# Kernel tuning notes

Measured on AMD Instinct MI355X. Metric: run time of the kernel, lower is better.

Reference implementation:

```python
import jax, jax.numpy as jnp
import numpy as np

N = 50000      # nodes
E = 800000     # edges
B = 512        # graphs in batch
DRNL = 64      # drnl_dim (feature_dim = 0)
H = 256        # hidden


def setup_inputs() -> dict:
    key = jax.random.key(0)
    ks = jax.random.split(key, 12)
    x = jax.random.normal(ks[0], (N, DRNL), jnp.float32)
    edge_index = jax.random.randint(ks[1], (2, E), 0, N)
    batch_vec = jnp.sort(jax.random.randint(ks[2], (N,), 0, B))
    u_idx = jax.random.randint(ks[3], (B,), 0, N)
    v_idx = jax.random.randint(ks[4], (B,), 0, N)

    def glorot(k, shp):
        scale = jnp.sqrt(2.0 / (shp[0] + shp[1]))
        return (jax.random.normal(k, shp, jnp.float32) * scale).astype(jnp.float32)

    W0 = glorot(ks[5], (DRNL, H)); b0 = jnp.zeros((H,), jnp.float32)
    W1 = glorot(ks[6], (H, H));    b1 = jnp.zeros((H,), jnp.float32)
    W2 = glorot(ks[7], (H, H));    b2 = jnp.zeros((H,), jnp.float32)
    Wm1 = glorot(ks[8], (3 * H, H)); bm1 = jnp.zeros((H,), jnp.float32)
    Wm2 = glorot(ks[9], (H, 1));     bm2 = jnp.zeros((1,), jnp.float32)
    return dict(x=x, edge_index=edge_index, batch_vec=batch_vec,
                u_idx=u_idx, v_idx=v_idx,
                W0=W0, b0=b0, W1=W1, b1=b1, W2=W2, b2=b2,
                Wm1=Wm1, bm1=bm1, Wm2=Wm2, bm2=bm2)


def _gcn_encode(x, src, dst, Ws, bs):
    # Standard GCN: h' = D^-1/2 (A + I) D^-1/2 h W + b, ReLU between layers.
    n = x.shape[0]
    loop = jnp.arange(n)
    src2 = jnp.concatenate([src, loop])  # add self-loops
    dst2 = jnp.concatenate([dst, loop])
    deg = jax.ops.segment_sum(jnp.ones_like(dst2, x.dtype), dst2, num_segments=n)
    dis = jax.lax.rsqrt(jnp.maximum(deg, 1.0))          # D^-1/2
    norm = dis[src2] * dis[dst2]                         # per-edge norm [E+N]

    h = x
    for i, (W, b) in enumerate(zip(Ws, bs)):
        msg = h[src2] * norm[:, None]                    # gather + scale
        agg = jax.ops.segment_sum(msg, dst2, num_segments=n)
        h = agg @ W + b
        if i < len(Ws) - 1:
            h = jax.nn.relu(h)
    return h


def reference(x, edge_index, batch_vec, u_idx, v_idx,
              W0, b0, W1, b1, W2, b2, Wm1, bm1, Wm2, bm2):
    src, dst = edge_index[0], edge_index[1]
    h = _gcn_encode(x, src, dst, (W0, W1, W2), (b0, b1, b2))   # [N, H]

    # global_mean_pool over batch_vec -> [B, H]
    cnt = jax.ops.segment_sum(jnp.ones((h.shape[0],), h.dtype), batch_vec,
                              num_segments=B)
    g = jax.ops.segment_sum(h, batch_vec, num_segments=B) / \
        jnp.maximum(cnt, 1.0)[:, None]

    # concat [g, h[u], h[v]] -> MLP -> [B] logits
    z = jnp.concatenate([g, h[u_idx], h[v_idx]], axis=1)       # [B, 3H]
    z = jax.nn.relu(z @ Wm1 + bm1)
    return (z @ Wm2 + bm2).squeeze(-1)
```

## Files before the change

kernel.cpp:

```cpp
#include <hip/hip_runtime.h>
#include <hip/hip_bf16.h>
#include <stdint.h>

#ifndef DRNL
#define DRNL 64
#define HDIM 256
#endif

#define CHUNK 4096
#define BCAP 3072

typedef __attribute__((ext_vector_type(4))) float f32x4;
typedef __attribute__((ext_vector_type(8))) _Float16 f16x8;

__device__ __forceinline__ void async16(void* lds, const void* g) {
    __builtin_amdgcn_global_load_lds(
        (const __attribute__((address_space(1))) void*)g,
        (__attribute__((address_space(3))) void*)(char*)lds, 16, 0, 0);
}

__device__ __forceinline__ int imin(int a, int b) { return a < b ? a : b; }

__global__ __launch_bounds__(256) void k_misc(
    const int* __restrict__ batch,
    const float* __restrict__ x,
    const float* __restrict__ W0, const float* __restrict__ W1,
    const float* __restrict__ W2,
    int* __restrict__ gstart,
    _Float16* __restrict__ x16,
    _Float16* __restrict__ W0t, _Float16* __restrict__ W1t,
    _Float16* __restrict__ W2t,
    int N, int B) {
    const int gsz = gridDim.x * 256;
    const int gid0 = blockIdx.x * 256 + threadIdx.x;

    for (int i = gid0; i < (DRNL + 2 * HDIM) * 256; i += gsz) {
        int b = i >> 8, c = i & 255;
        const float* W; _Float16* T; int k, K;
        if (b < DRNL)            { W = W0; T = W0t; k = b;              K = DRNL; }
        else if (b < DRNL + 256) { W = W1; T = W1t; k = b - DRNL;       K = HDIM; }
        else                     { W = W2; T = W2t; k = b - DRNL - 256; K = HDIM; }
        int KT = K >> 5;
        int cg = c >> 6, ct = (c >> 4) & 3, cl = c & 15;
        int kt = k >> 5, qq = (k >> 3) & 3, j = k & 7;
        int lane = (qq << 4) | cl;
        T[(((size_t)(cg * KT + kt) * 4 + ct) * 64 + lane) * 8 + j] =
            (_Float16)W[(size_t)k * 256 + c];
    }

    for (int i = gid0; i < N * DRNL; i += gsz) x16[i] = (_Float16)x[i];

    for (int i = gid0; i <= N; i += gsz) {
        if (i == 0) {
            int b0 = batch[0];
            for (int b = 0; b <= b0; ++b) gstart[b] = 0;
        } else if (i == N) {
            int bl = batch[N - 1];
            for (int b = bl + 1; b <= B; ++b) gstart[b] = N;
        } else {
            int bp = batch[i - 1], bc = batch[i];
            if (bc != bp)
                for (int b = bp + 1; b <= bc; ++b) gstart[b] = i;
        }
    }
}

__global__ __launch_bounds__(256) void k_hist(const int* __restrict__ dst,
                                              int* __restrict__ ghist,
                                              int E, int P, int SH, int NBUCK) {
    __shared__ int h[512];
    int tid = threadIdx.x, p = blockIdx.x;
    for (int i = tid; i < NBUCK; i += 256) h[i] = 0;
    __syncthreads();
    int e0 = p * CHUNK, e1 = imin(e0 + CHUNK, E);
    for (int e = e0 + tid; e < e1; e += 256)
        atomicAdd(&h[dst[e] >> SH], 1);
    __syncthreads();
    for (int b = tid; b < NBUCK; b += 256)
        ghist[(size_t)b * P + p] = h[b];
}

__global__ __launch_bounds__(256) void k_gbase(int* __restrict__ ghist,
                                               int* __restrict__ btot, int P) {
    __shared__ int s[256];
    int b = blockIdx.x, tid = threadIdx.x;
    int* row = ghist + (size_t)b * P;
    int carry = 0;
    for (int base = 0; base < P; base += 256) {
        int idx = base + tid;
        int v = (idx < P) ? row[idx] : 0;
        s[tid] = v;
        __syncthreads();
        for (int o = 1; o < 256; o <<= 1) {
            int t = (tid >= o) ? s[tid - o] : 0;
            __syncthreads();
            s[tid] += t;
            __syncthreads();
        }
        if (idx < P) row[idx] = carry + s[tid] - v;
        carry += s[255];
        __syncthreads();
    }
    if (tid == 0) btot[b] = carry;
}

__global__ __launch_bounds__(256) void k_btscan(const int* __restrict__ btot,
                                                int* __restrict__ bbase,
                                                int* __restrict__ rowptr,
                                                int NBUCK, int N, int E) {
    __shared__ int s[256];
    int tid = threadIdx.x;
    int carry = 0;
    for (int base = 0; base < NBUCK; base += 256) {
        int idx = base + tid;
        int v = (idx < NBUCK) ? btot[idx] : 0;
        s[tid] = v;
        __syncthreads();
        for (int o = 1; o < 256; o <<= 1) {
            int t = (tid >= o) ? s[tid - o] : 0;
            __syncthreads();
            s[tid] += t;
            __syncthreads();
        }
        if (idx < NBUCK) bbase[idx] = carry + s[tid] - v;
        carry += s[255];
        __syncthreads();
    }
    if (tid == 0) { bbase[NBUCK] = E; rowptr[N] = E; }
}

__global__ __launch_bounds__(256) void k_scatter(const int* __restrict__ src,
                                                 const int* __restrict__ dst,
                                                 const int* __restrict__ ghist,
                                                 const int* __restrict__ bbase,
                                                 int* __restrict__ tmp,
                                                 int E, int P, int SH, int NBUCK) {
    __shared__ int base[512];
    int p = blockIdx.x, tid = threadIdx.x;
    for (int b = tid; b < NBUCK; b += 256)
        base[b] = bbase[b] + ghist[(size_t)b * P + p];
    __syncthreads();
    int e0 = p * CHUNK, e1 = imin(e0 + CHUNK, E);
    int msk = (1 << SH) - 1;
    for (int e = e0 + tid; e < e1; e += 256) {
        int d = dst[e];
        int r = atomicAdd(&base[d >> SH], 1);
        tmp[r] = (src[e] << SH) | (d & msk);
    }
}

__global__ __launch_bounds__(256) void k_bsort(const int* __restrict__ tmp,
                                               const int* __restrict__ bbase,
                                               int* __restrict__ col,
                                               int* __restrict__ rowptr,
                                               float* __restrict__ dis,
                                               _Float16* __restrict__ x16,
                                               int SH, int N) {
    __shared__ int cnt[512];
    __shared__ int off[512];
    __shared__ int sscan[256];
    __shared__ int eL[BCAP];
    __shared__ unsigned short rnk[BCAP];
    __shared__ int sL[BCAP];
    int b = blockIdx.x, tid = threadIdx.x;
    int nodes = 1 << SH, node0 = b << SH, msk = nodes - 1;
    int lo = bbase[b], hi = bbase[b + 1], m = hi - lo;
    bool fast = (m <= BCAP);

    for (int i = tid; i < nodes; i += 256) cnt[i] = 0;
    __syncthreads();
    if (fast) {
        for (int i = tid; i < m; i += 256) {
            int v = tmp[lo + i];
            eL[i] = v;
            rnk[i] = (unsigned short)atomicAdd(&cnt[v & msk], 1);
        }
    } else {
        for (int i = tid; i < m; i += 256)
            atomicAdd(&cnt[tmp[lo + i] & msk], 1);
    }
    __syncthreads();
    int carry = 0;
    for (int base = 0; base < nodes; base += 256) {
        int idx = base + tid;
        int v = (idx < nodes) ? cnt[idx] : 0;
        sscan[tid] = v;
        __syncthreads();
        for (int o = 1; o < 256; o <<= 1) {
            int t = (tid >= o) ? sscan[tid - o] : 0;
            __syncthreads();
            sscan[tid] += t;
            __syncthreads();
        }
        if (idx < nodes) off[idx] = carry + sscan[tid] - v;
        carry += sscan[255];
        __syncthreads();
    }
    for (int i = tid; i < nodes; i += 256) {
        int node = node0 + i;
        if (node < N) {
            rowptr[node] = lo + off[i];
            dis[node]    = rsqrtf((float)cnt[i] + 1.f);
        }
    }
    int rlim = imin(nodes, N - node0);
    for (int u = tid; u < rlim * 8; u += 256) {
        int r = u >> 3, c = u & 7;
        float d = rsqrtf((float)cnt[r] + 1.f);
        f16x8* xv = (f16x8*)(x16 + (size_t)(node0 + r) * 64);
        f16x8 v = xv[c];
        f16x8 o;
#pragma unroll
        for (int k = 0; k < 8; ++k) o[k] = (_Float16)((float)v[k] * d);
        xv[c] = o;
    }
    __syncthreads();
    if (fast) {
        for (int i = tid; i < m; i += 256) {
            int v = eL[i];
            sL[off[v & msk] + rnk[i]] = v >> SH;
        }
        __syncthreads();
        for (int i = tid; i < m; i += 256) col[lo + i] = sL[i];
    } else {
        for (int i = tid; i < nodes; i += 256) cnt[i] = 0;
        __syncthreads();
        for (int i = tid; i < m; i += 256) {
            int v = tmp[lo + i];
            int d = v & msk;
            int r = atomicAdd(&cnt[d], 1);
            col[lo + off[d] + r] = v >> SH;
        }
    }
}

template <int FBLK>
__global__ __launch_bounds__(256) void k_agg(const _Float16* __restrict__ hs,
                                             const float* __restrict__ dis,
                                             const int* __restrict__ rowptr,
                                             const int* __restrict__ col,
                                             _Float16* __restrict__ A16, int N) {
    int node_wg, f;
    if constexpr (FBLK == 4) {
        int wg = blockIdx.x;
        int xcd = wg & 7;
        f = xcd >> 1;
        int half = xcd & 1;
        int NH = gridDim.x >> 3;
        node_wg = half * NH + (wg >> 3);
    } else {
        node_wg = blockIdx.x;
        f = 0;
    }
    int lane = threadIdx.x & 63;
    int wv = threadIdx.x >> 6;
    int oct = lane >> 3;
    int fl = lane & 7;
    int gw = node_wg * 32 + wv * 8 + oct;
    bool valid = gw < N;
    int gwc = valid ? gw : N - 1;
    const size_t boff = (size_t)f * ((size_t)N * 64);
    const f16x8* hv = (const f16x8*)(hs + boff);
    float acc[8];
#pragma unroll
    for (int k = 0; k < 8; ++k) acc[k] = 0.f;

    int e0 = rowptr[gwc];
    int e1 = valid ? rowptr[gwc + 1] : e0;
    int j = e0;
    while (__any(j < e1)) {
        bool a0 = j < e1, a1 = j + 1 < e1, a2 = j + 2 < e1, a3 = j + 3 < e1;
        int s0 = col[a0 ? j : 0];
        int s1 = col[a1 ? j + 1 : 0];
        int s2 = col[a2 ? j + 2 : 0];
        int s3 = col[a3 ? j + 3 : 0];
        float m0 = a0 ? 1.f : 0.f, m1 = a1 ? 1.f : 0.f;
        float m2 = a2 ? 1.f : 0.f, m3 = a3 ? 1.f : 0.f;
        f16x8 v0 = hv[(size_t)s0 * 8 + fl];
        f16x8 v1 = hv[(size_t)s1 * 8 + fl];
        f16x8 v2 = hv[(size_t)s2 * 8 + fl];
        f16x8 v3 = hv[(size_t)s3 * 8 + fl];
#pragma unroll
        for (int k = 0; k < 8; ++k) acc[k] += m0 * (float)v0[k];
#pragma unroll
        for (int k = 0; k < 8; ++k) acc[k] += m1 * (float)v1[k];
#pragma unroll
        for (int k = 0; k < 8; ++k) acc[k] += m2 * (float)v2[k];
#pragma unroll
        for (int k = 0; k < 8; ++k) acc[k] += m3 * (float)v3[k];
        j += 4;
    }

    float dn = dis[gwc];
    f16x8 hsv = hv[(size_t)gwc * 8 + fl];
    f16x8 o;
#pragma unroll
    for (int k = 0; k < 8; ++k)
        o[k] = (_Float16)((acc[k] + (float)hsv[k]) * dn);
    if (valid)
        __builtin_nontemporal_store(
            o, (f16x8*)(A16 + boff + (size_t)gw * 64 + fl * 8));
}

template <int K, int OUT_RELU, int SCALE>
__global__ __launch_bounds__(256, 1) void k_wgemm(const _Float16* __restrict__ A,
                                                  const _Float16* __restrict__ Wf,
                                                  const float* __restrict__ bias,
                                                  const float* __restrict__ dis,
                                                  _Float16* __restrict__ outh, int n) {
    constexpr int KT  = K / 32;
    constexpr int NFB = K / 64;
    constexpr int NI  = NFB * 2;
    constexpr int STG = NFB * 1024;
    __shared__ _Float16 sAll[4 * (STG + 1024)];

    const int tid  = threadIdx.x;
    const int lane = tid & 63;
    const int wv   = tid >> 6;
    const int c15  = lane & 15;
    const int q    = lane >> 4;
    const int row0 = blockIdx.x * 64;
    const size_t bstride = (size_t)n * 64;
    _Float16* sbuf = sAll + wv * (STG + 1024);
    _Float16* sO   = sbuf + STG;
    _Float16* ob   = outh + (size_t)wv * bstride;

    f16x8 wf[4][KT];
    const _Float16* wp = Wf + ((size_t)wv * KT * 4 * 64 + lane) * 8;
#pragma unroll
    for (int kt = 0; kt < KT; ++kt)
#pragma unroll
        for (int ct = 0; ct < 4; ++ct)
            wf[ct][kt] = *(const f16x8*)(wp + (size_t)((kt * 4 + ct) * 64) * 8);

    float bvl = bias[(wv << 6) + lane];
    float bv[4];
#pragma unroll
    for (int ct = 0; ct < 4; ++ct) bv[ct] = __shfl(bvl, (ct << 4) + c15);

    float dsv[4][4];
    if (SCALE) {
        float dvl = dis[imin(row0 + lane, n - 1)];
#pragma unroll
        for (int st = 0; st < 4; ++st)
#pragma unroll
            for (int r = 0; r < 4; ++r)
                dsv[st][r] = __shfl(dvl, (st << 4) + (q << 2) + r);
    }

#pragma unroll
    for (int st = 0; st < 4; ++st) {
        const int r0 = row0 + (st << 4);
#pragma unroll
        for (int i = 0; i < NI; ++i) {
            int s   = (i << 6) + lane;
            int fb  = s >> 7;
            int row = (s >> 3) & 15;
            int ch  = (s & 7) ^ (row & 7);
            int gr  = imin(r0 + row, n - 1);
            async16(sbuf + (size_t)s * 8,
                    A + (size_t)fb * bstride + (size_t)gr * 64 + ch * 8);
        }
        asm volatile("s_waitcnt vmcnt(0)" ::: "memory");
        __builtin_amdgcn_sched_barrier(0);

        f16x8 af[KT];
#pragma unroll
        for (int kt = 0; kt < KT; ++kt) {
            int off = (kt >> 1) * 1024 + c15 * 64 +
                      ((((kt & 1) * 4 + q) ^ (c15 & 7)) * 8);
            af[kt] = *(const f16x8*)(sbuf + off);
        }

        f32x4 acc[4];
#pragma unroll
        for (int ct = 0; ct < 4; ++ct) acc[ct] = (f32x4)0.f;
#pragma unroll
        for (int kt = 0; kt < KT; ++kt)
#pragma unroll
            for (int ct = 0; ct < 4; ++ct)
                acc[ct] = __builtin_amdgcn_mfma_f32_16x16x32_f16(
                    af[kt], wf[ct][kt], acc[ct], 0, 0, 0);

#pragma unroll
        for (int ct = 0; ct < 4; ++ct) {
#pragma unroll
            for (int r = 0; r < 4; ++r) {
                float v = acc[ct][r] + bv[ct];
                if (OUT_RELU) v = fmaxf(v, 0.f);
                if (SCALE) v *= dsv[st][r];
                int row = (q << 2) + r;
                int colx = (ct << 4) + c15;
                int sw = (((colx >> 3) ^ (row & 7)) << 3) | (colx & 7);
                sO[row * 64 + sw] = (_Float16)v;
            }
        }
#pragma unroll
        for (int ps = 0; ps < 2; ++ps) {
            int u = (ps << 6) + lane;
            int rr = u >> 3, ch2 = u & 7;
            f16x8 vv = *(const f16x8*)(sO + rr * 64 + ((ch2 ^ (rr & 7)) << 3));
            if (r0 + rr < n)
                *(f16x8*)(ob + (size_t)(r0 + rr) * 64 + ch2 * 8) = vv;
        }
    }
}

__global__ __launch_bounds__(256) void k_head(const _Float16* __restrict__ h,
                                              const int* __restrict__ gstart,
                                              const int* __restrict__ u,
                                              const int* __restrict__ v,
                                              const float* __restrict__ Wm1,
                                              const float* __restrict__ bm1,
                                              const float* __restrict__ Wm2,
                                              const float* __restrict__ bm2,
                                              float* __restrict__ out, int N) {
    int b = blockIdx.x;
    int t = threadIdx.x;
    __shared__ float z[3 * HDIM];
    __shared__ float red[4];
    const _Float16* hb = h + (size_t)(t >> 6) * ((size_t)N * 64) + (t & 63);
    int s = gstart[b], e = gstart[b + 1];
    float pa = 0.f;
    int i = s;
    for (; i + 3 < e; i += 4) {
        float a0 = (float)hb[(size_t)i * 64];
        float a1 = (float)hb[(size_t)(i + 1) * 64];
        float a2 = (float)hb[(size_t)(i + 2) * 64];
        float a3 = (float)hb[(size_t)(i + 3) * 64];
        pa += (a0 + a1) + (a2 + a3);
    }
    for (; i < e; ++i) pa += (float)hb[(size_t)i * 64];
    z[t]            = pa / fmaxf((float)(e - s), 1.f);
    z[HDIM + t]     = (float)hb[(size_t)u[b] * 64];
    z[2 * HDIM + t] = (float)hb[(size_t)v[b] * 64];
    __syncthreads();
    float acc[8];
#pragma unroll
    for (int k = 0; k < 8; ++k) acc[k] = 0.f;
    for (int k = 0; k < 3 * HDIM; k += 8) {
#pragma unroll
        for (int jj = 0; jj < 8; ++jj)
            acc[jj] = fmaf(z[k + jj], Wm1[(size_t)(k + jj) * HDIM + t], acc[jj]);
    }
    float sum = (((acc[0] + acc[1]) + (acc[2] + acc[3])) +
                 ((acc[4] + acc[5]) + (acc[6] + acc[7]))) + bm1[t];
    float hid = fmaxf(sum, 0.f);
    float p = hid * Wm2[t];
    for (int off = 32; off; off >>= 1) p += __shfl_down(p, off);
    if ((t & 63) == 0) red[t >> 6] = p;
    __syncthreads();
    if (t == 0) out[b] = red[0] + red[1] + red[2] + red[3] + bm2[0];
}

extern "C" void kernel_launch(void* const* d_in, const int* in_sizes, int n_in,
                              void* d_out, int out_size, void* d_ws, size_t ws_size,
                              hipStream_t stream) {
    const float* x    = (const float*)d_in[0];
    const int*   ei   = (const int*)d_in[1];
    const int*   batc = (const int*)d_in[2];
    const int*   uidx = (const int*)d_in[3];
    const int*   vidx = (const int*)d_in[4];
    const float* W0   = (const float*)d_in[5];
    const float* b0   = (const float*)d_in[6];
    const float* W1   = (const float*)d_in[7];
    const float* b1   = (const float*)d_in[8];
    const float* W2   = (const float*)d_in[9];
    const float* b2   = (const float*)d_in[10];
    const float* Wm1  = (const float*)d_in[11];
    const float* bm1  = (const float*)d_in[12];
    const float* Wm2  = (const float*)d_in[13];
    const float* bm2  = (const float*)d_in[14];
    float* out = (float*)d_out;

    const int N = in_sizes[0] / DRNL;
    const int E = in_sizes[1] / 2;
    const int B = in_sizes[3];
    const int* src = ei;
    const int* dst = ei + E;

    int SH = 7;
    while (((N + (1 << SH) - 1) >> SH) > 512) ++SH;
    const int NBUCK = (N + (1 << SH) - 1) >> SH;
    const int P = (E + CHUNK - 1) / CHUNK;

    char* w = (char*)d_ws;
    size_t off = 0;
    auto carve = [&](size_t bytes) {
        void* p = w + off;
        off = (off + bytes + 255) & ~(size_t)255;
        return p;
    };
    int*       rowptr = (int*)carve((size_t)(N + 1) * 4);
    int*       colA   = (int*)carve((size_t)E * 4);
    float*     dis    = (float*)carve((size_t)N * 4);
    int*       gstart = (int*)carve((size_t)(B + 1) * 4);
    _Float16*  A16    = (_Float16*)carve((size_t)N * HDIM * 2);
    _Float16*  h16    = (_Float16*)carve((size_t)N * HDIM * 2);
    _Float16*  x16    = (_Float16*)carve((size_t)N * DRNL * 2);
    _Float16*  W0t    = (_Float16*)carve((size_t)DRNL * HDIM * 2);
    _Float16*  W1t    = (_Float16*)carve((size_t)HDIM * HDIM * 2);
    _Float16*  W2t    = (_Float16*)carve((size_t)HDIM * HDIM * 2);
    int*       ghist  = (int*)carve((size_t)NBUCK * P * 4);
    int*       btot   = (int*)carve(512 * 4);
    int*       bbase  = (int*)carve(513 * 4);
    int*       tmpE   = (int*)carve((size_t)E * 4);
    (void)ws_size;

    k_misc<<<1024, 256, 0, stream>>>(batc, x, W0, W1, W2, gstart,
                                     x16, W0t, W1t, W2t, N, B);
    k_hist<<<P, 256, 0, stream>>>(dst, ghist, E, P, SH, NBUCK);
    k_gbase<<<NBUCK, 256, 0, stream>>>(ghist, btot, P);
    k_btscan<<<1, 256, 0, stream>>>(btot, bbase, rowptr, NBUCK, N, E);
    k_scatter<<<P, 256, 0, stream>>>(src, dst, ghist, bbase, tmpE, E, P, SH, NBUCK);
    k_bsort<<<NBUCK, 256, 0, stream>>>(tmpE, bbase, colA, rowptr, dis, x16, SH, N);

    int gemmb = (N + 63) / 64;
    int NB = (N + 31) / 32;
    int NH = (NB + 1) / 2;
    int aggb4 = 8 * NH;

    k_agg<1><<<NB, 256, 0, stream>>>(x16, dis, rowptr, colA, A16, N);
    k_wgemm<DRNL, 1, 1><<<gemmb, 256, 0, stream>>>(A16, W0t, b0, dis, h16, N);
    k_agg<4><<<aggb4, 256, 0, stream>>>(h16, dis, rowptr, colA, A16, N);
    k_wgemm<HDIM, 1, 1><<<gemmb, 256, 0, stream>>>(A16, W1t, b1, dis, h16, N);
    k_agg<4><<<aggb4, 256, 0, stream>>>(h16, dis, rowptr, colA, A16, N);
    k_wgemm<HDIM, 0, 0><<<gemmb, 256, 0, stream>>>(A16, W2t, b2, dis, h16, N);

    k_head<<<B, 256, 0, stream>>>(h16, gstart, uidx, vidx, Wm1, bm1, Wm2, bm2, out, N);
}
```

Baseline: 294.4 us.

## Fuse histogram into misc kernel, dynamic node scheduling in agg, double-buffer GEMM

Merges the edge histogram kernel into k_misc as extra blocks, removing one launch, and vectorizes the x-to-fp16 conversion to 16-byte loads and stores. The aggregation kernel now gives each workgroup 128 nodes and hands them out through an LDS atomic counter, so octets that finish short adjacency lists pick up new nodes instead of idling. The weight GEMM swaps its per-wave LDS staging for a shared double-buffered async load that prefetches the next 16-row stage while the current one is computed, and raises launch bounds to allow two blocks per CU. In exchange it adds barriers and atomics, and register pressure may grow under the new occupancy target.

```diff
diff --git a/kernel.cpp b/kernel.cpp
--- a/kernel.cpp
+++ b/kernel.cpp
@@ -30,9 +30,28 @@
     _Float16* __restrict__ x16,
     _Float16* __restrict__ W0t, _Float16* __restrict__ W1t,
     _Float16* __restrict__ W2t,
+    const int* __restrict__ dst, int* __restrict__ ghist,
+    int E, int P, int SH, int NBUCK,
     int N, int B) {
-    const int gsz = gridDim.x * 256;
-    const int gid0 = blockIdx.x * 256 + threadIdx.x;
+    const int tid = threadIdx.x;
+
+    if (blockIdx.x < P) {
+        __shared__ int h[512];
+        int p = blockIdx.x;
+        for (int i = tid; i < NBUCK; i += 256) h[i] = 0;
+        __syncthreads();
+        int e0 = p * CHUNK, e1 = imin(e0 + CHUNK, E);
+        for (int e = e0 + tid; e < e1; e += 256)
+            atomicAdd(&h[dst[e] >> SH], 1);
+        __syncthreads();
+        for (int b = tid; b < NBUCK; b += 256)
+            ghist[(size_t)b * P + p] = h[b];
+        return;
+    }
+
+    const int bid  = blockIdx.x - P;
+    const int gsz  = (gridDim.x - P) * 256;
+    const int gid0 = bid * 256 + tid;
 
     for (int i = gid0; i < (DRNL + 2 * HDIM) * 256; i += gsz) {
         int b = i >> 8, c = i & 255;
@@ -48,7 +67,20 @@
             (_Float16)W[(size_t)k * 256 + c];
     }
 
-    for (int i = gid0; i < N * DRNL; i += gsz) x16[i] = (_Float16)x[i];
+    {
+        const float4* x4 = (const float4*)x;
+        f16x8* xv = (f16x8*)x16;
+        int tot = N * DRNL / 8;
+        for (int i = gid0; i < tot; i += gsz) {
+            float4 a = x4[2 * i], b2 = x4[2 * i + 1];
+            f16x8 o;
+            o[0] = (_Float16)a.x;  o[1] = (_Float16)a.y;
+            o[2] = (_Float16)a.z;  o[3] = (_Float16)a.w;
+            o[4] = (_Float16)b2.x; o[5] = (_Float16)b2.y;
+            o[6] = (_Float16)b2.z; o[7] = (_Float16)b2.w;
+            xv[i] = o;
+        }
+    }
 
     for (int i = gid0; i <= N; i += gsz) {
         if (i == 0) {
@@ -63,21 +95,6 @@
                 for (int b = bp + 1; b <= bc; ++b) gstart[b] = i;
         }
     }
-}
-
-__global__ __launch_bounds__(256) void k_hist(const int* __restrict__ dst,
-                                              int* __restrict__ ghist,
-                                              int E, int P, int SH, int NBUCK) {
-    __shared__ int h[512];
-    int tid = threadIdx.x, p = blockIdx.x;
-    for (int i = tid; i < NBUCK; i += 256) h[i] = 0;
-    __syncthreads();
-    int e0 = p * CHUNK, e1 = imin(e0 + CHUNK, E);
-    for (int e = e0 + tid; e < e1; e += 256)
-        atomicAdd(&h[dst[e] >> SH], 1);
-    __syncthreads();
-    for (int b = tid; b < NBUCK; b += 256)
-        ghist[(size_t)b * P + p] = h[b];
 }
 
 __global__ __launch_bounds__(256) void k_gbase(int* __restrict__ ghist,
@@ -240,6 +257,7 @@
                                              const int* __restrict__ rowptr,
                                              const int* __restrict__ col,
                                              _Float16* __restrict__ A16, int N) {
+    __shared__ int cur;
     int node_wg, f;
     if constexpr (FBLK == 4) {
         int wg = blockIdx.x;
@@ -252,67 +270,85 @@
         node_wg = blockIdx.x;
         f = 0;
     }
-    int lane = threadIdx.x & 63;
-    int wv = threadIdx.x >> 6;
-    int oct = lane >> 3;
-    int fl = lane & 7;
-    int gw = node_wg * 32 + wv * 8 + oct;
-    bool valid = gw < N;
-    int gwc = valid ? gw : N - 1;
+    if (threadIdx.x == 0) cur = 32;
+    __syncthreads();
+    const int base = node_wg * 128;
+    const int lim  = imin(128, N - base);
+    if (lim <= 0) return;
+    const int lane  = threadIdx.x & 63;
+    const int fl    = lane & 7;
+    const int obase = lane & 56;
     const size_t boff = (size_t)f * ((size_t)N * 64);
     const f16x8* hv = (const f16x8*)(hs + boff);
+
+    int myn = threadIdx.x >> 3;
+    bool active = myn < lim;
+    int gn = base + (active ? myn : 0);
+    int j = 0, e1 = 0;
+    if (active) { j = rowptr[gn]; e1 = rowptr[gn + 1]; }
     float acc[8];
 #pragma unroll
     for (int k = 0; k < 8; ++k) acc[k] = 0.f;
 
-    int e0 = rowptr[gwc];
-    int e1 = valid ? rowptr[gwc + 1] : e0;
-    int j = e0;
-    while (__any(j < e1)) {
-        bool a0 = j < e1, a1 = j + 1 < e1, a2 = j + 2 < e1, a3 = j + 3 < e1;
-        int s0 = col[a0 ? j : 0];
-        int s1 = col[a1 ? j + 1 : 0];
-        int s2 = col[a2 ? j + 2 : 0];
-        int s3 = col[a3 ? j + 3 : 0];
-        float m0 = a0 ? 1.f : 0.f, m1 = a1 ? 1.f : 0.f;
-        float m2 = a2 ? 1.f : 0.f, m3 = a3 ? 1.f : 0.f;
-        f16x8 v0 = hv[(size_t)s0 * 8 + fl];
-        f16x8 v1 = hv[(size_t)s1 * 8 + fl];
-        f16x8 v2 = hv[(size_t)s2 * 8 + fl];
-        f16x8 v3 = hv[(size_t)s3 * 8 + fl];
-#pragma unroll
-        for (int k = 0; k < 8; ++k) acc[k] += m0 * (float)v0[k];
-#pragma unroll
-        for (int k = 0; k < 8; ++k) acc[k] += m1 * (float)v1[k];
-#pragma unroll
-        for (int k = 0; k < 8; ++k) acc[k] += m2 * (float)v2[k];
-#pragma unroll
-        for (int k = 0; k < 8; ++k) acc[k] += m3 * (float)v3[k];
-        j += 4;
-    }
-
-    float dn = dis[gwc];
-    f16x8 hsv = hv[(size_t)gwc * 8 + fl];
-    f16x8 o;
-#pragma unroll
-    for (int k = 0; k < 8; ++k)
-        o[k] = (_Float16)((acc[k] + (float)hsv[k]) * dn);
-    if (valid)
-        __builtin_nontemporal_store(
-            o, (f16x8*)(A16 + boff + (size_t)gw * 64 + fl * 8));
+    while (__any(active)) {
+        if (active) {
+            bool a0 = j < e1, a1 = j + 1 < e1, a2 = j + 2 < e1, a3 = j + 3 < e1;
+            int s0 = col[a0 ? j : 0];
+            int s1 = col[a1 ? j + 1 : 0];
+            int s2 = col[a2 ? j + 2 : 0];
+            int s3 = col[a3 ? j + 3 : 0];
+            float m0 = a0 ? 1.f : 0.f, m1 = a1 ? 1.f : 0.f;
+            float m2 = a2 ? 1.f : 0.f, m3 = a3 ? 1.f : 0.f;
+            f16x8 v0 = hv[(size_t)s0 * 8 + fl];
+            f16x8 v1 = hv[(size_t)s1 * 8 + fl];
+            f16x8 v2 = hv[(size_t)s2 * 8 + fl];
+            f16x8 v3 = hv[(size_t)s3 * 8 + fl];
+#pragma unroll
+            for (int k = 0; k < 8; ++k) acc[k] += m0 * (float)v0[k];
+#pragma unroll
+            for (int k = 0; k < 8; ++k) acc[k] += m1 * (float)v1[k];
+#pragma unroll
+            for (int k = 0; k < 8; ++k) acc[k] += m2 * (float)v2[k];
+#pragma unroll
+            for (int k = 0; k < 8; ++k) acc[k] += m3 * (float)v3[k];
+            j += 4;
+            if (j >= e1) {
+                float dn = dis[gn];
+                f16x8 hsv = hv[(size_t)gn * 8 + fl];
+                f16x8 o;
+#pragma unroll
+                for (int k = 0; k < 8; ++k)
+                    o[k] = (_Float16)((acc[k] + (float)hsv[k]) * dn);
+                __builtin_nontemporal_store(
+                    o, (f16x8*)(A16 + boff + (size_t)gn * 64 + fl * 8));
+#pragma unroll
+                for (int k = 0; k < 8; ++k) acc[k] = 0.f;
+                int nn = 0;
+                if (fl == 0) nn = atomicAdd(&cur, 1);
+                nn = __shfl(nn, obase);
+                if (nn < lim) {
+                    myn = nn; gn = base + myn;
+                    j = rowptr[gn]; e1 = rowptr[gn + 1];
+                } else {
+                    active = false;
+                }
+            }
+        }
+    }
 }
 
 template <int K, int OUT_RELU, int SCALE>
-__global__ __launch_bounds__(256, 1) void k_wgemm(const _Float16* __restrict__ A,
+__global__ __launch_bounds__(256, 2) void k_wgemm(const _Float16* __restrict__ A,
                                                   const _Float16* __restrict__ Wf,
                                                   const float* __restrict__ bias,
                                                   const float* __restrict__ dis,
                                                   _Float16* __restrict__ outh, int n) {
-    constexpr int KT  = K / 32;
-    constexpr int NFB = K / 64;
-    constexpr int NI  = NFB * 2;
-    constexpr int STG = NFB * 1024;
-    __shared__ _Float16 sAll[4 * (STG + 1024)];
+    constexpr int KT    = K / 32;
+    constexpr int CPR   = K / 8;
+    constexpr int SLOTS = 16 * CPR;
+    constexpr int SHW   = 16 * K;
+    __shared__ _Float16 sA[2 * SHW];
+    __shared__ _Float16 sOut[4 * 16 * 64];
 
     const int tid  = threadIdx.x;
     const int lane = tid & 63;
@@ -321,9 +357,28 @@
     const int q    = lane >> 4;
     const int row0 = blockIdx.x * 64;
     const size_t bstride = (size_t)n * 64;
-    _Float16* sbuf = sAll + wv * (STG + 1024);
-    _Float16* sO   = sbuf + STG;
-    _Float16* ob   = outh + (size_t)wv * bstride;
+    _Float16* sO = sOut + wv * (16 * 64);
+    _Float16* ob = outh + (size_t)wv * bstride;
+
+    auto stage = [&](int b, int st) {
+        const int r0 = row0 + (st << 4);
+        _Float16* dstp = sA + b * SHW;
+#pragma unroll
+        for (int i = 0; i < (SLOTS + 255) / 256; ++i) {
+            int s = (i << 8) + tid;
+            if (SLOTS % 256 == 0 || s < SLOTS) {
+                int row = s / CPR;
+                int chs = s % CPR;
+                int cg  = chs ^ (row & 7);
+                int gr  = imin(r0 + row, n - 1);
+                async16(dstp + (size_t)s * 8,
+                        A + (size_t)(cg >> 3) * bstride + (size_t)gr * 64 +
+                            (cg & 7) * 8);
+            }
+        }
+    };
+
+    stage(0, 0);
 
     f16x8 wf[4][KT];
     const _Float16* wp = Wf + ((size_t)wv * KT * 4 * 64 + lane) * 8;
@@ -348,28 +403,20 @@
                 dsv[st][r] = __shfl(dvl, (st << 4) + (q << 2) + r);
     }
 
+    asm volatile("s_waitcnt vmcnt(0)" ::: "memory");
+    __builtin_amdgcn_sched_barrier(0);
+    __builtin_amdgcn_s_barrier();
+
 #pragma unroll
     for (int st = 0; st < 4; ++st) {
-        const int r0 = row0 + (st << 4);
-#pragma unroll
-        for (int i = 0; i < NI; ++i) {
-            int s   = (i << 6) + lane;
-            int fb  = s >> 7;
-            int row = (s >> 3) & 15;
-            int ch  = (s & 7) ^ (row & 7);
-            int gr  = imin(r0 + row, n - 1);
-            async16(sbuf + (size_t)s * 8,
-                    A + (size_t)fb * bstride + (size_t)gr * 64 + ch * 8);
-        }
-        asm volatile("s_waitcnt vmcnt(0)" ::: "memory");
-        __builtin_amdgcn_sched_barrier(0);
-
+        if (st < 3) stage((st + 1) & 1, st + 1);
+
+        const _Float16* buf = sA + (st & 1) * SHW;
         f16x8 af[KT];
 #pragma unroll
         for (int kt = 0; kt < KT; ++kt) {
-            int off = (kt >> 1) * 1024 + c15 * 64 +
-                      ((((kt & 1) * 4 + q) ^ (c15 & 7)) * 8);
-            af[kt] = *(const f16x8*)(sbuf + off);
+            int cg = kt * 4 + q;
+            af[kt] = *(const f16x8*)(buf + c15 * K + ((cg ^ (c15 & 7)) * 8));
         }
 
         f32x4 acc[4];
@@ -382,6 +429,7 @@
                 acc[ct] = __builtin_amdgcn_mfma_f32_16x16x32_f16(
                     af[kt], wf[ct][kt], acc[ct], 0, 0, 0);
 
+        const int r0 = row0 + (st << 4);
 #pragma unroll
         for (int ct = 0; ct < 4; ++ct) {
 #pragma unroll
@@ -402,6 +450,12 @@
             f16x8 vv = *(const f16x8*)(sO + rr * 64 + ((ch2 ^ (rr & 7)) << 3));
             if (r0 + rr < n)
                 *(f16x8*)(ob + (size_t)(r0 + rr) * 64 + ch2 * 8) = vv;
+        }
+
+        if (st < 3) {
+            asm volatile("s_waitcnt vmcnt(2)" ::: "memory");
+            __builtin_amdgcn_sched_barrier(0);
+            __builtin_amdgcn_s_barrier();
         }
     }
 }
@@ -507,20 +561,20 @@
     int*       tmpE   = (int*)carve((size_t)E * 4);
     (void)ws_size;
 
-    k_misc<<<1024, 256, 0, stream>>>(batc, x, W0, W1, W2, gstart,
-                                     x16, W0t, W1t, W2t, N, B);
-    k_hist<<<P, 256, 0, stream>>>(dst, ghist, E, P, SH, NBUCK);
+    k_misc<<<P + 1024, 256, 0, stream>>>(batc, x, W0, W1, W2, gstart,
+                                         x16, W0t, W1t, W2t,
+                                         dst, ghist, E, P, SH, NBUCK, N, B);
     k_gbase<<<NBUCK, 256, 0, stream>>>(ghist, btot, P);
     k_btscan<<<1, 256, 0, stream>>>(btot, bbase, rowptr, NBUCK, N, E);
     k_scatter<<<P, 256, 0, stream>>>(src, dst, ghist, bbase, tmpE, E, P, SH, NBUCK);
     k_bsort<<<NBUCK, 256, 0, stream>>>(tmpE, bbase, colA, rowptr, dis, x16, SH, N);
 
     int gemmb = (N + 63) / 64;
-    int NB = (N + 31) / 32;
-    int NH = (NB + 1) / 2;
+    int NB128 = (N + 127) / 128;
+    int NH = (NB128 + 1) / 2;
     int aggb4 = 8 * NH;
 
-    k_agg<1><<<NB, 256, 0, stream>>>(x16, dis, rowptr, colA, A16, N);
+    k_agg<1><<<NB128, 256, 0, stream>>>(x16, dis, rowptr, colA, A16, N);
     k_wgemm<DRNL, 1, 1><<<gemmb, 256, 0, stream>>>(A16, W0t, b0, dis, h16, N);
     k_agg<4><<<aggb4, 256, 0, stream>>>(h16, dis, rowptr, colA, A16, N);
     k_wgemm<HDIM, 1, 1><<<gemmb, 256, 0, stream>>>(A16, W1t, b1, dis, h16, N);
```

Result: slower. 322.6 us (+9.6%).

## Merge histogram into misc kernel, vectorize x cast, unroll gather by 8

Applied to the files above, without the earlier changes.

Folds the dst-bucket histogram kernel into the misc preprocessing kernel as extra leading blocks, removing one launch and letting the two independent jobs run side by side. The fp32-to-fp16 conversion of x is vectorised to move eight elements per thread iteration. The aggregation loop now issues eight neighbour gathers per step instead of four, for more memory-level parallelism. The cost is higher register use and more masked wasted loads on low-degree nodes.

```diff
diff --git a/kernel.cpp b/kernel.cpp
--- a/kernel.cpp
+++ b/kernel.cpp
@@ -30,9 +30,28 @@
     _Float16* __restrict__ x16,
     _Float16* __restrict__ W0t, _Float16* __restrict__ W1t,
     _Float16* __restrict__ W2t,
+    const int* __restrict__ dst, int* __restrict__ ghist,
+    int E, int P, int SH, int NBUCK,
     int N, int B) {
-    const int gsz = gridDim.x * 256;
-    const int gid0 = blockIdx.x * 256 + threadIdx.x;
+    const int tid = threadIdx.x;
+
+    if (blockIdx.x < P) {
+        __shared__ int h[512];
+        int p = blockIdx.x;
+        for (int i = tid; i < NBUCK; i += 256) h[i] = 0;
+        __syncthreads();
+        int e0 = p * CHUNK, e1 = imin(e0 + CHUNK, E);
+        for (int e = e0 + tid; e < e1; e += 256)
+            atomicAdd(&h[dst[e] >> SH], 1);
+        __syncthreads();
+        for (int b = tid; b < NBUCK; b += 256)
+            ghist[(size_t)b * P + p] = h[b];
+        return;
+    }
+
+    const int bid  = blockIdx.x - P;
+    const int gsz  = (gridDim.x - P) * 256;
+    const int gid0 = bid * 256 + tid;
 
     for (int i = gid0; i < (DRNL + 2 * HDIM) * 256; i += gsz) {
         int b = i >> 8, c = i & 255;
@@ -48,7 +67,20 @@
             (_Float16)W[(size_t)k * 256 + c];
     }
 
-    for (int i = gid0; i < N * DRNL; i += gsz) x16[i] = (_Float16)x[i];
+    {
+        const float4* x4 = (const float4*)x;
+        f16x8* xv = (f16x8*)x16;
+        int tot = N * DRNL / 8;
+        for (int i = gid0; i < tot; i += gsz) {
+            float4 a = x4[2 * i], b2 = x4[2 * i + 1];
+            f16x8 o;
+            o[0] = (_Float16)a.x;  o[1] = (_Float16)a.y;
+            o[2] = (_Float16)a.z;  o[3] = (_Float16)a.w;
+            o[4] = (_Float16)b2.x; o[5] = (_Float16)b2.y;
+            o[6] = (_Float16)b2.z; o[7] = (_Float16)b2.w;
+            xv[i] = o;
+        }
+    }
 
     for (int i = gid0; i <= N; i += gsz) {
         if (i == 0) {
@@ -63,21 +95,6 @@
                 for (int b = bp + 1; b <= bc; ++b) gstart[b] = i;
         }
     }
-}
-
-__global__ __launch_bounds__(256) void k_hist(const int* __restrict__ dst,
-                                              int* __restrict__ ghist,
-                                              int E, int P, int SH, int NBUCK) {
-    __shared__ int h[512];
-    int tid = threadIdx.x, p = blockIdx.x;
-    for (int i = tid; i < NBUCK; i += 256) h[i] = 0;
-    __syncthreads();
-    int e0 = p * CHUNK, e1 = imin(e0 + CHUNK, E);
-    for (int e = e0 + tid; e < e1; e += 256)
-        atomicAdd(&h[dst[e] >> SH], 1);
-    __syncthreads();
-    for (int b = tid; b < NBUCK; b += 256)
-        ghist[(size_t)b * P + p] = h[b];
 }
 
 __global__ __launch_bounds__(256) void k_gbase(int* __restrict__ ghist,
@@ -269,26 +286,24 @@
     int e1 = valid ? rowptr[gwc + 1] : e0;
     int j = e0;
     while (__any(j < e1)) {
-        bool a0 = j < e1, a1 = j + 1 < e1, a2 = j + 2 < e1, a3 = j + 3 < e1;
-        int s0 = col[a0 ? j : 0];
-        int s1 = col[a1 ? j + 1 : 0];
-        int s2 = col[a2 ? j + 2 : 0];
-        int s3 = col[a3 ? j + 3 : 0];
-        float m0 = a0 ? 1.f : 0.f, m1 = a1 ? 1.f : 0.f;
-        float m2 = a2 ? 1.f : 0.f, m3 = a3 ? 1.f : 0.f;
-        f16x8 v0 = hv[(size_t)s0 * 8 + fl];
-        f16x8 v1 = hv[(size_t)s1 * 8 + fl];
-        f16x8 v2 = hv[(size_t)s2 * 8 + fl];
-        f16x8 v3 = hv[(size_t)s3 * 8 + fl];
-#pragma unroll
-        for (int k = 0; k < 8; ++k) acc[k] += m0 * (float)v0[k];
-#pragma unroll
-        for (int k = 0; k < 8; ++k) acc[k] += m1 * (float)v1[k];
-#pragma unroll
-        for (int k = 0; k < 8; ++k) acc[k] += m2 * (float)v2[k];
-#pragma unroll
-        for (int k = 0; k < 8; ++k) acc[k] += m3 * (float)v3[k];
-        j += 4;
+        int   idx[8];
+        float mm[8];
+        f16x8 vv[8];
+#pragma unroll
+        for (int u = 0; u < 8; ++u) {
+            bool a = (j + u) < e1;
+            idx[u] = col[a ? j + u : 0];
+            mm[u]  = a ? 1.f : 0.f;
+        }
+#pragma unroll
+        for (int u = 0; u < 8; ++u)
+            vv[u] = hv[(size_t)idx[u] * 8 + fl];
+#pragma unroll
+        for (int u = 0; u < 8; ++u)
+#pragma unroll
+            for (int k = 0; k < 8; ++k)
+                acc[k] += mm[u] * (float)vv[u][k];
+        j += 8;
     }
 
     float dn = dis[gwc];
@@ -507,9 +522,9 @@
     int*       tmpE   = (int*)carve((size_t)E * 4);
     (void)ws_size;
 
-    k_misc<<<1024, 256, 0, stream>>>(batc, x, W0, W1, W2, gstart,
-                                     x16, W0t, W1t, W2t, N, B);
-    k_hist<<<P, 256, 0, stream>>>(dst, ghist, E, P, SH, NBUCK);
+    k_misc<<<P + 1024, 256, 0, stream>>>(batc, x, W0, W1, W2, gstart,
+                                         x16, W0t, W1t, W2t,
+                                         dst, ghist, E, P, SH, NBUCK, N, B);
     k_gbase<<<NBUCK, 256, 0, stream>>>(ghist, btot, P);
     k_btscan<<<1, 256, 0, stream>>>(btot, bbase, rowptr, NBUCK, N, E);
     k_scatter<<<P, 256, 0, stream>>>(src, dst, ghist, bbase, tmpE, E, P, SH, NBUCK);
```

Result: slower. 304.9 us (+3.6%).
